# Kernel optimization log

Hardware: AMD Instinct MI355X
Metric: run time of the kernel (lower is better)

Reference implementation:

```python
import jax, jax.numpy as jnp
import numpy as np

CUTOFF = 5.0
NLINKED = 1
CELL_LIST = CUTOFF / NLINKED  # linked-cell edge length
_r = np.arange(-NLINKED, NLINKED + 1)
# torch.cartesian_prod(r1,r1,r1) == meshgrid(indexing='ij') stacked & flattened
LINKED = np.stack(np.meshgrid(_r, _r, _r, indexing='ij'), axis=-1).reshape(1, -1, 3).astype(np.float32)  # (1, 27, 3)


def setup_inputs() -> dict:
    N = 2744
    L = 30.0
    key = jax.random.key(0)
    k1, k2 = jax.random.split(key)
    coordinates = jax.random.uniform(k1, (N, 3), dtype=jnp.float32) * L
    cell = jnp.eye(3, dtype=jnp.float32) * L
    mass = jax.random.uniform(k2, (N,), dtype=jnp.float32) * 15.0 + 1.0
    period_table = jnp.ones((3,), dtype=jnp.int32)  # fully periodic
    return {"period_table": period_table, "coordinates": coordinates, "cell": cell, "mass": mass}


def _forward(period_table, coordinates, cell, mass):
    numatom = coordinates.shape[0]
    # wrap coordinates into the cell relative to atom 0 (fractional coords)
    inv_cell = jnp.linalg.inv(cell)
    inv_coor = coordinates @ inv_cell
    inv_coor = inv_coor - jnp.round(inv_coor - inv_coor[0])
    coordinates = inv_coor @ cell
    # remove center of mass
    com = (mass @ coordinates) / jnp.sum(mass)
    coordinates = coordinates - com[None, :]
    # periodic replicas needed to cover the cutoff
    num_repeats = jnp.ceil(jnp.min(CUTOFF / jnp.abs(cell), axis=0)).astype(jnp.int32)
    num_repeats = period_table.astype(jnp.int32) * num_repeats
    up = num_repeats + 1
    down = -num_repeats
    rs = [jnp.arange(int(down[i]), int(up[i])) for i in range(3)]
    g = jnp.meshgrid(*rs, indexing='ij')
    shifts_frac = jnp.stack(g, axis=-1).reshape(-1, 3).astype(coordinates.dtype)  # (S, 3)
    shifts = shifts_frac @ cell  # (S, 3) cartesian shift vectors
    num_shifts = shifts.shape[0]
    # prod = cartesian_prod(all_shifts, all_atoms).T : row0 shift idx, row1 atom idx
    prod0 = jnp.repeat(jnp.arange(num_shifts), numatom)
    prod1 = jnp.tile(jnp.arange(numatom), num_shifts)
    # shift box so all coords are positive; pad by cutoff
    mincoor = jnp.min(coordinates, axis=0) - CUTOFF - 1e-6
    coordinates = coordinates - mincoor
    maxcoor = jnp.max(coordinates, axis=0) + CUTOFF
    # all periodic images, keep only those inside the padded box
    image = (coordinates[None, :, :] + shifts[:, None, :]).reshape(-1, 3)
    keep = jnp.nonzero(((image < maxcoor) & (image > 0)).all(axis=1))[0]
    image_mask = image[keep]                      # (M, 3)
    prod0 = prod0[keep]
    prod1 = prod1[keep]
    # linked-cell indices
    ori_image_index = jnp.floor(coordinates / CELL_LIST)         # (N, 3)
    neigh_cell = ori_image_index[:, None, :] + jnp.asarray(LINKED)  # (N, 27, 3)
    image_index = jnp.floor(image_mask / CELL_LIST)              # (M, 3)
    max_cell_index = jnp.ceil(maxcoor / CELL_LIST)
    f10 = max_cell_index[1] * max_cell_index[0]
    neigh_cell_index = neigh_cell[:, :, 2] * f10 + neigh_cell[:, :, 1] * max_cell_index[0] + neigh_cell[:, :, 0]  # (N, 27)
    nimage_index = image_index[:, 2] * f10 + image_index[:, 1] * max_cell_index[0] + image_index[:, 0]            # (M,)
    # dense (N, M, 27) cell-index equality -- the memory-bound hot spot
    eq = neigh_cell_index[:, None, :] == nimage_index[None, :, None]
    ai, aj, _ = jnp.nonzero(eq)
    # distance filter on candidate pairs
    d = jnp.linalg.norm(coordinates[ai] - image_mask[aj], axis=-1)
    pair = jnp.nonzero((d < CUTOFF) & (d > 0.001))[0]
    center = ai[pair]
    img = aj[pair]
    shift_idx = prod0[img]
    atom_j = prod1[img]
    neigh_list = jnp.stack([center, atom_j])  # (2, P)
    return neigh_list, shifts[shift_idx], shifts_frac, shift_idx


def reference(period_table, coordinates, cell, mass):
    neigh_list, shifts_out, _, _ = _forward(period_table, coordinates, cell, mass)
    return (neigh_list, shifts_out)
```

## Files before the change

### kernel.cpp

```cpp
#include <hip/hip_runtime.h>
#include <math.h>

#define S_CAP     27
#define NCELL_MAX 1024
#define CAP       64
#define CAPSH     6
#define MAXNB     128
#define CUT       5.0f
#define K1T       1024


__global__ __launch_bounds__(K1T)
void k1_pre(const int* __restrict__ period, const float* __restrict__ coor,
            const float* __restrict__ cell, const float* __restrict__ mass,
            int* hdr_i, float* hdr_f, float* shifts, float* xv,
            int* __restrict__ ccur, int n)
{
    #pragma clang fp contract(off)
    __shared__ double wsum[16][4];
    __shared__ float  wred[16][6];
    int t = threadIdx.x;

    for (int c = t; c < NCELL_MAX; c += K1T) ccur[c] = 0;

    float c[3][3];
    #pragma unroll
    for (int i = 0; i < 3; i++)
        #pragma unroll
        for (int j = 0; j < 3; j++) c[i][j] = cell[3 * i + j];

    float a00 = c[1][1]*c[2][2] - c[1][2]*c[2][1];
    float a01 = c[0][2]*c[2][1] - c[0][1]*c[2][2];
    float a02 = c[0][1]*c[1][2] - c[0][2]*c[1][1];
    float a10 = c[1][2]*c[2][0] - c[1][0]*c[2][2];
    float a11 = c[0][0]*c[2][2] - c[0][2]*c[2][0];
    float a12 = c[0][2]*c[1][0] - c[0][0]*c[1][2];
    float a20 = c[1][0]*c[2][1] - c[1][1]*c[2][0];
    float a21 = c[0][1]*c[2][0] - c[0][0]*c[2][1];
    float a22 = c[0][0]*c[1][1] - c[0][1]*c[1][0];
    float det = c[0][0]*a00 + c[0][1]*a10 + c[0][2]*a20;
    float inv[3][3] = {{a00/det, a01/det, a02/det},
                       {a10/det, a11/det, a12/det},
                       {a20/det, a21/det, a22/det}};

    float f0[3];
    #pragma unroll
    for (int d = 0; d < 3; d++)
        f0[d] = coor[0]*inv[0][d] + coor[1]*inv[1][d] + coor[2]*inv[2][d];

    double sm = 0.0, sx = 0.0, sy = 0.0, sz = 0.0;
    float mn0 =  __builtin_inff(), mn1 =  __builtin_inff(), mn2 =  __builtin_inff();
    float mx0 = -__builtin_inff(), mx1 = -__builtin_inff(), mx2 = -__builtin_inff();
    for (int i = t; i < n; i += K1T) {
        float p0 = coor[3*i], p1 = coor[3*i+1], p2 = coor[3*i+2];
        float ic[3], w[3], x[3];
        #pragma unroll
        for (int d = 0; d < 3; d++)
            ic[d] = p0*inv[0][d] + p1*inv[1][d] + p2*inv[2][d];
        #pragma unroll
        for (int d = 0; d < 3; d++)
            w[d] = ic[d] - rintf(ic[d] - f0[d]);
        #pragma unroll
        for (int d = 0; d < 3; d++)
            x[d] = w[0]*c[0][d] + w[1]*c[1][d] + w[2]*c[2][d];
        xv[3*i] = x[0]; xv[3*i+1] = x[1]; xv[3*i+2] = x[2];
        float m = mass[i];
        sm += (double)m;
        sx += (double)m * (double)x[0];
        sy += (double)m * (double)x[1];
        sz += (double)m * (double)x[2];
        mn0 = fminf(mn0, x[0]); mn1 = fminf(mn1, x[1]); mn2 = fminf(mn2, x[2]);
        mx0 = fmaxf(mx0, x[0]); mx1 = fmaxf(mx1, x[1]); mx2 = fmaxf(mx2, x[2]);
    }
    #pragma unroll
    for (int off = 32; off > 0; off >>= 1) {
        sm += __shfl_down(sm, off, 64);
        sx += __shfl_down(sx, off, 64);
        sy += __shfl_down(sy, off, 64);
        sz += __shfl_down(sz, off, 64);
        mn0 = fminf(mn0, __shfl_down(mn0, off, 64));
        mn1 = fminf(mn1, __shfl_down(mn1, off, 64));
        mn2 = fminf(mn2, __shfl_down(mn2, off, 64));
        mx0 = fmaxf(mx0, __shfl_down(mx0, off, 64));
        mx1 = fmaxf(mx1, __shfl_down(mx1, off, 64));
        mx2 = fmaxf(mx2, __shfl_down(mx2, off, 64));
    }
    if ((t & 63) == 0) {
        int wv = t >> 6;
        wsum[wv][0] = sm; wsum[wv][1] = sx; wsum[wv][2] = sy; wsum[wv][3] = sz;
        wred[wv][0] = mn0; wred[wv][1] = mn1; wred[wv][2] = mn2;
        wred[wv][3] = mx0; wred[wv][4] = mx1; wred[wv][5] = mx2;
    }
    __syncthreads();
    if (t == 0) {
        double SM = 0.0, SX = 0.0, SY = 0.0, SZ = 0.0;
        float MN0 =  __builtin_inff(), MN1 =  __builtin_inff(), MN2 =  __builtin_inff();
        float MX0 = -__builtin_inff(), MX1 = -__builtin_inff(), MX2 = -__builtin_inff();
        #pragma unroll
        for (int q = 0; q < 16; q++) {
            SM += wsum[q][0]; SX += wsum[q][1]; SY += wsum[q][2]; SZ += wsum[q][3];
            MN0 = fminf(MN0, wred[q][0]); MN1 = fminf(MN1, wred[q][1]); MN2 = fminf(MN2, wred[q][2]);
            MX0 = fmaxf(MX0, wred[q][3]); MX1 = fmaxf(MX1, wred[q][4]); MX2 = fmaxf(MX2, wred[q][5]);
        }
        float den  = (float)SM;
        float com0 = ((float)SX) / den;
        float com1 = ((float)SY) / den;
        float com2 = ((float)SZ) / den;
        float m20 = ((MN0 - com0) - CUT) - 1e-6f;
        float m21 = ((MN1 - com1) - CUT) - 1e-6f;
        float m22 = ((MN2 - com2) - CUT) - 1e-6f;
        float maxc0 = ((MX0 - com0) - m20) + CUT;
        float maxc1 = ((MX1 - com1) - m21) + CUT;
        float maxc2 = ((MX2 - com2) - m22) + CUT;
        float mcell0 = ceilf(maxc0 / CUT);
        float mcell1 = ceilf(maxc1 / CUT);
        float f10 = mcell1 * mcell0;
        int nr[3];
        for (int j = 0; j < 3; j++) {
            float v = __builtin_inff();
            for (int i = 0; i < 3; i++) {
                float q = CUT / fabsf(c[i][j]);
                v = fminf(v, q);
            }
            nr[j] = (int)ceilf(v);
            nr[j] *= period[j];
        }
        int nsz0 = 2*nr[0]+1, nsz1 = 2*nr[1]+1, nsz2 = 2*nr[2]+1;
        int S = nsz0 * nsz1 * nsz2;
        if (S > S_CAP) S = S_CAP;
        hdr_i[0] = S;
        hdr_i[3] = -nr[0]; hdr_i[4] = -nr[1]; hdr_i[5] = -nr[2];
        hdr_i[6] = nsz0;   hdr_i[7] = nsz1;   hdr_i[8] = nsz2;
        hdr_i[9]  = (int)mcell0;
        hdr_i[10] = (int)f10;
        hdr_f[0] = maxc0; hdr_f[1] = maxc1; hdr_f[2] = maxc2;
        hdr_f[3] = f10;   hdr_f[4] = mcell0;
        hdr_f[5] = m20;   hdr_f[6] = m21;   hdr_f[7] = m22;
        hdr_f[8] = com0;  hdr_f[9] = com1;  hdr_f[10] = com2;
    }
    __syncthreads();
    int S = hdr_i[0];
    if (t < S) {
        int n1 = hdr_i[7], n2 = hdr_i[8];
        int i0 = t / (n1 * n2);
        int rem = t - i0 * n1 * n2;
        int i1 = rem / n2;
        int i2 = rem - i1 * n2;
        float fx = (float)(hdr_i[3] + i0);
        float fy = (float)(hdr_i[4] + i1);
        float fz = (float)(hdr_i[5] + i2);
        #pragma unroll
        for (int d = 0; d < 3; d++)
            shifts[3*t + d] = fx*c[0][d] + fy*c[1][d] + fz*c[2][d];
    }
}

__global__ __launch_bounds__(256)
void k2_fill(const int* __restrict__ hdr_i, const float* __restrict__ hdr_f,
             const float* __restrict__ shifts, const float* __restrict__ xv,
             int* __restrict__ ccur, float4* __restrict__ cellbuf, int n)
{
    #pragma clang fp contract(off)
    int a = blockIdx.x * 256 + threadIdx.x;
    int s = blockIdx.y;
    if (a >= n || s >= hdr_i[0]) return;
    float m20 = hdr_f[5], m21 = hdr_f[6], m22 = hdr_f[7];
    float com0 = hdr_f[8], com1 = hdr_f[9], com2 = hdr_f[10];
    float u0 = (xv[3*a]   - com0) - m20;
    float u1 = (xv[3*a+1] - com1) - m21;
    float u2 = (xv[3*a+2] - com2) - m22;
    float i0 = u0 + shifts[3*s];
    float i1 = u1 + shifts[3*s+1];
    float i2 = u2 + shifts[3*s+2];
    bool k = (i0 > 0.0f) && (i0 < hdr_f[0]) &&
             (i1 > 0.0f) && (i1 < hdr_f[1]) &&
             (i2 > 0.0f) && (i2 < hdr_f[2]);
    if (!k) return;
    float fc0 = floorf(i0 / CUT);
    float fc1 = floorf(i1 / CUT);
    float fc2 = floorf(i2 / CUT);
    float cf = fc2 * hdr_f[3] + fc1 * hdr_f[4] + fc0;
    int ci = (int)cf;
    if ((unsigned)ci >= (unsigned)NCELL_MAX) return;
    int pos = atomicAdd(&ccur[ci], 1);
    if (pos < CAP)
        cellbuf[(ci << CAPSH) + pos] = make_float4(i0, i1, i2, __int_as_float(s * n + a));
}

__global__ __launch_bounds__(256)
void k3_search(const int* __restrict__ hdr_i, const float* __restrict__ hdr_f,
               const float* __restrict__ xv, const int* __restrict__ ccur,
               const float4* __restrict__ cellbuf, int* __restrict__ nb,
               int* __restrict__ npair, int n)
{
    #pragma clang fp contract(off)
    int t    = threadIdx.x;
    int lane = t & 63;
    int w    = t >> 6;
    int atom = blockIdx.x * 4 + w;
    if (atom >= n) return;

    float m20 = hdr_f[5], m21 = hdr_f[6], m22 = hdr_f[7];
    float com0 = hdr_f[8], com1 = hdr_f[9], com2 = hdr_f[10];
    int mci = hdr_i[9], f10i = hdr_i[10];
    float x0 = (xv[3*atom]   - com0) - m20;
    float x1 = (xv[3*atom+1] - com1) - m21;
    float x2 = (xv[3*atom+2] - com2) - m22;
    int o0 = (int)floorf(x0 / CUT);
    int o1 = (int)floorf(x1 / CUT);
    int o2 = (int)floorf(x2 / CUT);

    int ncb[9], c0a[9], c1a[9], cum[10];
    cum[0] = 0;
    #pragma unroll
    for (int r = 0; r < 9; r++) {
        int dz = r / 3 - 1, dy = r % 3 - 1;
        ncb[r] = (o2+dz)*f10i + (o1+dy)*mci + (o0-1);
        int q0 = 0, q1 = 0, q2 = 0, nc;
        nc = ncb[r];     if ((unsigned)nc < (unsigned)NCELL_MAX) { q0 = ccur[nc]; q0 = q0 > CAP ? CAP : q0; }
        nc = ncb[r] + 1; if ((unsigned)nc < (unsigned)NCELL_MAX) { q1 = ccur[nc]; q1 = q1 > CAP ? CAP : q1; }
        nc = ncb[r] + 2; if ((unsigned)nc < (unsigned)NCELL_MAX) { q2 = ccur[nc]; q2 = q2 > CAP ? CAP : q2; }
        c0a[r] = q0; c1a[r] = q1;
        cum[r+1] = cum[r] + q0 + q1 + q2;
    }
    int T = cum[9];
    int cnt = 0;
    int* slab = nb + (size_t)atom * MAXNB;
    for (int base = 0; base < T; base += 64) {
        int L = base + lane;
        bool act = L < T;
        bool ok = false; int g = 0;
        if (act) {
            int r = 0;
            #pragma unroll
            for (int q = 1; q < 9; q++) r += (L >= cum[q]) ? 1 : 0;
            int off = L - cum[r];
            int c0 = c0a[r], c1 = c1a[r];
            int slot = (off < c0)      ? ((ncb[r]     << CAPSH) + off)
                     : (off < c0 + c1) ? (((ncb[r]+1) << CAPSH) + off - c0)
                                       : (((ncb[r]+2) << CAPSH) + off - c0 - c1);
            float4 v = cellbuf[slot];
            g = __float_as_int(v.w);
            float dxx = x0 - v.x;
            float dyy = x1 - v.y;
            float dzz = x2 - v.z;
            float ss = dxx*dxx + dyy*dyy + dzz*dzz;
            float dd = sqrtf(ss);
            ok = (dd < CUT) && (dd > 0.001f);
        }
        unsigned long long m = __ballot(ok);
        int posn = cnt + (int)__popcll(m & ((1ull << lane) - 1ull));
        if (ok && posn < MAXNB) slab[posn] = g;
        cnt += (int)__popcll(m);
    }
    if (cnt > MAXNB) cnt = MAXNB;
    if (lane == 0) npair[atom] = cnt;
}

__global__ __launch_bounds__(256)
void k4_emit(const int* __restrict__ nb, const int* __restrict__ npair,
             const float* __restrict__ shifts, float* __restrict__ out,
             int n, int P)
{
    __shared__ int si[256];
    __shared__ int lst[4][MAXNB];
    __shared__ int s_np[4];
    int t    = threadIdx.x;
    int lane = t & 63;
    int w    = t >> 6;
    int blk  = blockIdx.x;
    int atom = blk * 4 + w;
    bool valid = atom < n;

    int lim = blk * 4;
    int s = 0;
    for (int i = t; i < lim; i += 256) s += npair[i];
    si[t] = s;
    __syncthreads();
    for (int off = 128; off > 0; off >>= 1) {
        if (t < off) si[t] += si[t + off];
        __syncthreads();
    }
    int prefB = si[0];

    int cnt = 0;
    if (valid) {
        cnt = npair[atom];
        if (cnt > MAXNB) cnt = MAXNB;
        if (lane == 0) s_np[w] = cnt;
        const int* slab = nb + (size_t)atom * MAXNB;
        for (int r = lane; r < cnt; r += 64) lst[w][r] = slab[r];
    } else if (lane == 0) {
        s_np[w] = 0;
    }
    __syncthreads();

    if (valid) {
        int base = prefB;
        for (int q = 0; q < w; q++) base += s_np[q];
        for (int r = lane; r < cnt; r += 64) {
            int g = lst[w][r];
            int rank = 0;
            for (int q = 0; q < cnt; q++) rank += (lst[w][q] < g) ? 1 : 0;
            int p = base + rank;
            if (p < P) {
                int sidx = g / n;
                int a = g - sidx * n;
                out[p]     = (float)atom;
                out[P + p] = (float)a;
                out[2*P + 3*p]     = shifts[3*sidx];
                out[2*P + 3*p + 1] = shifts[3*sidx + 1];
                out[2*P + 3*p + 2] = shifts[3*sidx + 2];
            }
        }
    }
}

extern "C" void kernel_launch(void* const* d_in, const int* in_sizes, int n_in,
                              void* d_out, int out_size, void* d_ws, size_t ws_size,
                              hipStream_t stream)
{
    const int*   period = (const int*)d_in[0];
    const float* coor   = (const float*)d_in[1];
    const float* cell   = (const float*)d_in[2];
    const float* mass   = (const float*)d_in[3];
    float* out = (float*)d_out;

    int n = in_sizes[1] / 3;
    int P = out_size / 5;

    char* wp = (char*)d_ws;
    size_t off = 0;
    auto alloc = [&](size_t bytes) -> void* {
        off = (off + 15) & ~(size_t)15;
        void* pp = (void*)(wp + off); off += bytes; return pp;
    };

    int*    hdr_i   = (int*)   alloc(16 * 4);
    float*  hdr_f   = (float*) alloc(16 * 4);
    float*  shifts  = (float*) alloc(3 * S_CAP * 4);
    float*  xv      = (float*) alloc(3 * (size_t)n * 4);
    int*    ccur    = (int*)   alloc(NCELL_MAX * 4);
    float4* cellbuf = (float4*)alloc((size_t)NCELL_MAX * CAP * 16);
    int*    nb      = (int*)   alloc((size_t)n * MAXNB * 4);
    int*    npair   = (int*)   alloc((size_t)n * 4);
    (void)ws_size; (void)n_in;

    int gb_atom = (n + 3) / 4;
    dim3 g2((n + 255) / 256, S_CAP);

    hipLaunchKernelGGL(k1_pre,    dim3(1),       dim3(K1T), 0, stream,
                       period, coor, cell, mass, hdr_i, hdr_f, shifts, xv, ccur, n);
    hipLaunchKernelGGL(k2_fill,   g2,            dim3(256), 0, stream,
                       hdr_i, hdr_f, shifts, xv, ccur, cellbuf, n);
    hipLaunchKernelGGL(k3_search, dim3(gb_atom), dim3(256), 0, stream,
                       hdr_i, hdr_f, xv, ccur, cellbuf, nb, npair, n);
    hipLaunchKernelGGL(k4_emit,   dim3(gb_atom), dim3(256), 0, stream,
                       nb, npair, shifts, out, n, P);
}
```

Before: 87.46 us.

## Fuse preprocessing into cell-fill kernel with redundant per-block reductions

Merges the single-block preprocessing kernel into the cell-fill kernel. Every block now recomputes the wrapped coordinates, the center-of-mass and min/max reductions over all atoms, and the shift vectors itself. Block (0,0) still writes the header and the shift table for later kernels. The wrapped-coordinate buffer is removed, the search kernel recomputes atom wrapping from the raw inputs, and the counter reset moves to a memset. This removes one serial single-block launch and its dependency, at the cost of redundant O(N) reduction work in each of roughly 297 blocks, plus a memset call.

Result: slower. 89.74 us (+2.6%).

```diff
diff --git a/kernel.cpp b/kernel.cpp
--- a/kernel.cpp
+++ b/kernel.cpp
@@ -7,21 +7,66 @@
 #define CAPSH     6
 #define MAXNB     128
 #define CUT       5.0f
-#define K1T       1024
-
-
-__global__ __launch_bounds__(K1T)
-void k1_pre(const int* __restrict__ period, const float* __restrict__ coor,
-            const float* __restrict__ cell, const float* __restrict__ mass,
-            int* hdr_i, float* hdr_f, float* shifts, float* xv,
-            int* __restrict__ ccur, int n)
+
+
+struct Hdr {
+    float com0, com1, com2, m20, m21, m22, maxc0, maxc1, maxc2;
+    float mcell0, f10;
+    int   S, nsz1, nsz2, dn0, dn1, dn2, mci, f10i;
+};
+
+__device__ inline Hdr make_hdr(double SM, double SX, double SY, double SZ,
+                               float MN0, float MN1, float MN2,
+                               float MX0, float MX1, float MX2,
+                               const float c[3][3], const int* period)
 {
     #pragma clang fp contract(off)
-    __shared__ double wsum[16][4];
-    __shared__ float  wred[16][6];
+    Hdr h;
+    float den = (float)SM;
+    h.com0 = ((float)SX) / den;
+    h.com1 = ((float)SY) / den;
+    h.com2 = ((float)SZ) / den;
+    h.m20 = ((MN0 - h.com0) - CUT) - 1e-6f;
+    h.m21 = ((MN1 - h.com1) - CUT) - 1e-6f;
+    h.m22 = ((MN2 - h.com2) - CUT) - 1e-6f;
+    h.maxc0 = ((MX0 - h.com0) - h.m20) + CUT;
+    h.maxc1 = ((MX1 - h.com1) - h.m21) + CUT;
+    h.maxc2 = ((MX2 - h.com2) - h.m22) + CUT;
+    h.mcell0 = ceilf(h.maxc0 / CUT);
+    float mcell1 = ceilf(h.maxc1 / CUT);
+    h.f10 = mcell1 * h.mcell0;
+    int nr[3];
+    for (int j = 0; j < 3; j++) {
+        float v = __builtin_inff();
+        for (int i = 0; i < 3; i++) {
+            float q = CUT / fabsf(c[i][j]);
+            v = fminf(v, q);
+        }
+        nr[j] = (int)ceilf(v);
+        nr[j] *= period[j];
+    }
+    int nsz0 = 2*nr[0]+1; h.nsz1 = 2*nr[1]+1; h.nsz2 = 2*nr[2]+1;
+    int S = nsz0 * h.nsz1 * h.nsz2;
+    if (S > S_CAP) S = S_CAP;
+    h.S = S;
+    h.dn0 = -nr[0]; h.dn1 = -nr[1]; h.dn2 = -nr[2];
+    h.mci  = (int)h.mcell0;
+    h.f10i = (int)h.f10;
+    return h;
+}
+
+__global__ __launch_bounds__(256)
+void k12_fill(const int* __restrict__ period, const float* __restrict__ coor,
+              const float* __restrict__ cell, const float* __restrict__ mass,
+              int* hdr_i, float* hdr_f, float* shifts,
+              int* __restrict__ ccur, float4* __restrict__ cellbuf, int n)
+{
+    #pragma clang fp contract(off)
+    __shared__ double wsum[4][4];
+    __shared__ float  wred[4][6];
     int t = threadIdx.x;
-
-    for (int c = t; c < NCELL_MAX; c += K1T) ccur[c] = 0;
+    int lane = t & 63;
+    int wv = t >> 6;
 
     float c[3][3];
     #pragma unroll
@@ -51,7 +96,10 @@
     double sm = 0.0, sx = 0.0, sy = 0.0, sz = 0.0;
     float mn0 =  __builtin_inff(), mn1 =  __builtin_inff(), mn2 =  __builtin_inff();
     float mx0 = -__builtin_inff(), mx1 = -__builtin_inff(), mx2 = -__builtin_inff();
-    for (int i = t; i < n; i += K1T) {
+    float ax0 = 0.f, ax1 = 0.f, ax2 = 0.f;
+    bool hasatom = false;
+    int k = 0;
+    for (int i = t; i < n; i += 256, k++) {
         float p0 = coor[3*i], p1 = coor[3*i+1], p2 = coor[3*i+2];
         float ic[3], w[3], x[3];
         #pragma unroll
@@ -63,7 +111,7 @@
         #pragma unroll
         for (int d = 0; d < 3; d++)
             x[d] = w[0]*c[0][d] + w[1]*c[1][d] + w[2]*c[2][d];
-        xv[3*i] = x[0]; xv[3*i+1] = x[1]; xv[3*i+2] = x[2];
+        if (k == (int)blockIdx.x) { ax0 = x[0]; ax1 = x[1]; ax2 = x[2]; hasatom = true; }
         float m = mass[i];
         sm += (double)m;
         sx += (double)m * (double)x[0];
@@ -85,113 +133,88 @@
         mx1 = fmaxf(mx1, __shfl_down(mx1, off, 64));
         mx2 = fmaxf(mx2, __shfl_down(mx2, off, 64));
     }
-    if ((t & 63) == 0) {
-        int wv = t >> 6;
+    if (lane == 0) {
         wsum[wv][0] = sm; wsum[wv][1] = sx; wsum[wv][2] = sy; wsum[wv][3] = sz;
         wred[wv][0] = mn0; wred[wv][1] = mn1; wred[wv][2] = mn2;
         wred[wv][3] = mx0; wred[wv][4] = mx1; wred[wv][5] = mx2;
     }
     __syncthreads();
-    if (t == 0) {
-        double SM = 0.0, SX = 0.0, SY = 0.0, SZ = 0.0;
-        float MN0 =  __builtin_inff(), MN1 =  __builtin_inff(), MN2 =  __builtin_inff();
-        float MX0 = -__builtin_inff(), MX1 = -__builtin_inff(), MX2 = -__builtin_inff();
-        #pragma unroll
-        for (int q = 0; q < 16; q++) {
-            SM += wsum[q][0]; SX += wsum[q][1]; SY += wsum[q][2]; SZ += wsum[q][3];
-            MN0 = fminf(MN0, wred[q][0]); MN1 = fminf(MN1, wred[q][1]); MN2 = fminf(MN2, wred[q][2]);
-            MX0 = fmaxf(MX0, wred[q][3]); MX1 = fmaxf(MX1, wred[q][4]); MX2 = fmaxf(MX2, wred[q][5]);
+    double SM = 0.0, SX = 0.0, SY = 0.0, SZ = 0.0;
+    float MN0 =  __builtin_inff(), MN1 =  __builtin_inff(), MN2 =  __builtin_inff();
+    float MX0 = -__builtin_inff(), MX1 = -__builtin_inff(), MX2 = -__builtin_inff();
+    #pragma unroll
+    for (int q = 0; q < 4; q++) {
+        SM += wsum[q][0]; SX += wsum[q][1]; SY += wsum[q][2]; SZ += wsum[q][3];
+        MN0 = fminf(MN0, wred[q][0]); MN1 = fminf(MN1, wred[q][1]); MN2 = fminf(MN2, wred[q][2]);
+        MX0 = fmaxf(MX0, wred[q][3]); MX1 = fmaxf(MX1, wred[q][4]); MX2 = fmaxf(MX2, wred[q][5]);
+    }
+    Hdr h = make_hdr(SM, SX, SY, SZ, MN0, MN1, MN2, MX0, MX1, MX2, c, period);
+
+    if (blockIdx.x == 0 && blockIdx.y == 0) {
+        if (t == 0) {
+            hdr_i[0] = h.S;
+            hdr_i[3] = h.dn0; hdr_i[4] = h.dn1; hdr_i[5] = h.dn2;
+            hdr_i[7] = h.nsz1; hdr_i[8] = h.nsz2;
+            hdr_i[9]  = h.mci;
+            hdr_i[10] = h.f10i;
+            hdr_f[0] = h.maxc0; hdr_f[1] = h.maxc1; hdr_f[2] = h.maxc2;
+            hdr_f[3] = h.f10;   hdr_f[4] = h.mcell0;
+            hdr_f[5] = h.m20;   hdr_f[6] = h.m21;   hdr_f[7] = h.m22;
+            hdr_f[8] = h.com0;  hdr_f[9] = h.com1;  hdr_f[10] = h.com2;
         }
-        float den  = (float)SM;
-        float com0 = ((float)SX) / den;
-        float com1 = ((float)SY) / den;
-        float com2 = ((float)SZ) / den;
-        float m20 = ((MN0 - com0) - CUT) - 1e-6f;
-        float m21 = ((MN1 - com1) - CUT) - 1e-6f;
-        float m22 = ((MN2 - com2) - CUT) - 1e-6f;
-        float maxc0 = ((MX0 - com0) - m20) + CUT;
-        float maxc1 = ((MX1 - com1) - m21) + CUT;
-        float maxc2 = ((MX2 - com2) - m22) + CUT;
-        float mcell0 = ceilf(maxc0 / CUT);
-        float mcell1 = ceilf(maxc1 / CUT);
-        float f10 = mcell1 * mcell0;
-        int nr[3];
-        for (int j = 0; j < 3; j++) {
-            float v = __builtin_inff();
-            for (int i = 0; i < 3; i++) {
-                float q = CUT / fabsf(c[i][j]);
-                v = fminf(v, q);
-            }
-            nr[j] = (int)ceilf(v);
-            nr[j] *= period[j];
+        if (t < h.S) {
+            int i0 = t / (h.nsz1 * h.nsz2);
+            int rem = t - i0 * h.nsz1 * h.nsz2;
+            int i1 = rem / h.nsz2;
+            int i2 = rem - i1 * h.nsz2;
+            float fx = (float)(h.dn0 + i0);
+            float fy = (float)(h.dn1 + i1);
+            float fz = (float)(h.dn2 + i2);
+            #pragma unroll
+            for (int d = 0; d < 3; d++)
+                shifts[3*t + d] = fx*c[0][d] + fy*c[1][d] + fz*c[2][d];
         }
-        int nsz0 = 2*nr[0]+1, nsz1 = 2*nr[1]+1, nsz2 = 2*nr[2]+1;
-        int S = nsz0 * nsz1 * nsz2;
-        if (S > S_CAP) S = S_CAP;
-        hdr_i[0] = S;
-        hdr_i[3] = -nr[0]; hdr_i[4] = -nr[1]; hdr_i[5] = -nr[2];
-        hdr_i[6] = nsz0;   hdr_i[7] = nsz1;   hdr_i[8] = nsz2;
-        hdr_i[9]  = (int)mcell0;
-        hdr_i[10] = (int)f10;
-        hdr_f[0] = maxc0; hdr_f[1] = maxc1; hdr_f[2] = maxc2;
-        hdr_f[3] = f10;   hdr_f[4] = mcell0;
-        hdr_f[5] = m20;   hdr_f[6] = m21;   hdr_f[7] = m22;
-        hdr_f[8] = com0;  hdr_f[9] = com1;  hdr_f[10] = com2;
-    }
-    __syncthreads();
-    int S = hdr_i[0];
-    if (t < S) {
-        int n1 = hdr_i[7], n2 = hdr_i[8];
-        int i0 = t / (n1 * n2);
-        int rem = t - i0 * n1 * n2;
-        int i1 = rem / n2;
-        int i2 = rem - i1 * n2;
-        float fx = (float)(hdr_i[3] + i0);
-        float fy = (float)(hdr_i[4] + i1);
-        float fz = (float)(hdr_i[5] + i2);
-        #pragma unroll
-        for (int d = 0; d < 3; d++)
-            shifts[3*t + d] = fx*c[0][d] + fy*c[1][d] + fz*c[2][d];
-    }
-}
-
-__global__ __launch_bounds__(256)
-void k2_fill(const int* __restrict__ hdr_i, const float* __restrict__ hdr_f,
-             const float* __restrict__ shifts, const float* __restrict__ xv,
-             int* __restrict__ ccur, float4* __restrict__ cellbuf, int n)
-{
-    #pragma clang fp contract(off)
-    int a = blockIdx.x * 256 + threadIdx.x;
+    }
+
     int s = blockIdx.y;
-    if (a >= n || s >= hdr_i[0]) return;
-    float m20 = hdr_f[5], m21 = hdr_f[6], m22 = hdr_f[7];
-    float com0 = hdr_f[8], com1 = hdr_f[9], com2 = hdr_f[10];
-    float u0 = (xv[3*a]   - com0) - m20;
-    float u1 = (xv[3*a+1] - com1) - m21;
-    float u2 = (xv[3*a+2] - com2) - m22;
-    float i0 = u0 + shifts[3*s];
-    float i1 = u1 + shifts[3*s+1];
-    float i2 = u2 + shifts[3*s+2];
-    bool k = (i0 > 0.0f) && (i0 < hdr_f[0]) &&
-             (i1 > 0.0f) && (i1 < hdr_f[1]) &&
-             (i2 > 0.0f) && (i2 < hdr_f[2]);
-    if (!k) return;
+    if (!hasatom || s >= h.S) return;
+    int i0s = s / (h.nsz1 * h.nsz2);
+    int rem = s - i0s * h.nsz1 * h.nsz2;
+    int i1s = rem / h.nsz2;
+    int i2s = rem - i1s * h.nsz2;
+    float fx = (float)(h.dn0 + i0s);
+    float fy = (float)(h.dn1 + i1s);
+    float fz = (float)(h.dn2 + i2s);
+    float sh0 = fx*c[0][0] + fy*c[1][0] + fz*c[2][0];
+    float sh1 = fx*c[0][1] + fy*c[1][1] + fz*c[2][1];
+    float sh2 = fx*c[0][2] + fy*c[1][2] + fz*c[2][2];
+    float u0 = (ax0 - h.com0) - h.m20;
+    float u1 = (ax1 - h.com1) - h.m21;
+    float u2 = (ax2 - h.com2) - h.m22;
+    float i0 = u0 + sh0;
+    float i1 = u1 + sh1;
+    float i2 = u2 + sh2;
+    bool kk = (i0 > 0.0f) && (i0 < h.maxc0) &&
+              (i1 > 0.0f) && (i1 < h.maxc1) &&
+              (i2 > 0.0f) && (i2 < h.maxc2);
+    if (!kk) return;
     float fc0 = floorf(i0 / CUT);
     float fc1 = floorf(i1 / CUT);
     float fc2 = floorf(i2 / CUT);
-    float cf = fc2 * hdr_f[3] + fc1 * hdr_f[4] + fc0;
+    float cf = fc2 * h.f10 + fc1 * h.mcell0 + fc0;
     int ci = (int)cf;
     if ((unsigned)ci >= (unsigned)NCELL_MAX) return;
+    int a = blockIdx.x * 256 + t;
     int pos = atomicAdd(&ccur[ci], 1);
     if (pos < CAP)
         cellbuf[(ci << CAPSH) + pos] = make_float4(i0, i1, i2, __int_as_float(s * n + a));
 }
 
 __global__ __launch_bounds__(256)
-void k3_search(const int* __restrict__ hdr_i, const float* __restrict__ hdr_f,
-               const float* __restrict__ xv, const int* __restrict__ ccur,
-               const float4* __restrict__ cellbuf, int* __restrict__ nb,
-               int* __restrict__ npair, int n)
+void k3_search(const float* __restrict__ coor, const float* __restrict__ cell,
+               const int* __restrict__ hdr_i, const float* __restrict__ hdr_f,
+               const int* __restrict__ ccur, const float4* __restrict__ cellbuf,
+               int* __restrict__ nb, int* __restrict__ npair, int n)
 {
     #pragma clang fp contract(off)
     int t    = threadIdx.x;
@@ -200,12 +223,47 @@
     int atom = blockIdx.x * 4 + w;
     if (atom >= n) return;
 
+    float c[3][3];
+    #pragma unroll
+    for (int i = 0; i < 3; i++)
+        #pragma unroll
+        for (int j = 0; j < 3; j++) c[i][j] = cell[3 * i + j];
+    float a00 = c[1][1]*c[2][2] - c[1][2]*c[2][1];
+    float a01 = c[0][2]*c[2][1] - c[0][1]*c[2][2];
+    float a02 = c[0][1]*c[1][2] - c[0][2]*c[1][1];
+    float a10 = c[1][2]*c[2][0] - c[1][0]*c[2][2];
+    float a11 = c[0][0]*c[2][2] - c[0][2]*c[2][0];
+    float a12 = c[0][2]*c[1][0] - c[0][0]*c[1][2];
+    float a20 = c[1][0]*c[2][1] - c[1][1]*c[2][0];
+    float a21 = c[0][1]*c[2][0] - c[0][0]*c[2][1];
+    float a22 = c[0][0]*c[1][1] - c[0][1]*c[1][0];
+    float det = c[0][0]*a00 + c[0][1]*a10 + c[0][2]*a20;
+    float inv[3][3] = {{a00/det, a01/det, a02/det},
+                       {a10/det, a11/det, a12/det},
+                       {a20/det, a21/det, a22/det}};
+    float f0[3];
+    #pragma unroll
+    for (int d = 0; d < 3; d++)
+        f0[d] = coor[0]*inv[0][d] + coor[1]*inv[1][d] + coor[2]*inv[2][d];
+
+    float p0 = coor[3*atom], p1 = coor[3*atom+1], p2 = coor[3*atom+2];
+    float ic[3], ww[3], x[3];
+    #pragma unroll
+    for (int d = 0; d < 3; d++)
+        ic[d] = p0*inv[0][d] + p1*inv[1][d] + p2*inv[2][d];
+    #pragma unroll
+    for (int d = 0; d < 3; d++)
+        ww[d] = ic[d] - rintf(ic[d] - f0[d]);
+    #pragma unroll
+    for (int d = 0; d < 3; d++)
+        x[d] = ww[0]*c[0][d] + ww[1]*c[1][d] + ww[2]*c[2][d];
+
     float m20 = hdr_f[5], m21 = hdr_f[6], m22 = hdr_f[7];
     float com0 = hdr_f[8], com1 = hdr_f[9], com2 = hdr_f[10];
     int mci = hdr_i[9], f10i = hdr_i[10];
-    float x0 = (xv[3*atom]   - com0) - m20;
-    float x1 = (xv[3*atom+1] - com1) - m21;
-    float x2 = (xv[3*atom+2] - com2) - m22;
+    float x0 = (x[0] - com0) - m20;
+    float x1 = (x[1] - com1) - m21;
+    float x2 = (x[2] - com2) - m22;
     int o0 = (int)floorf(x0 / CUT);
     int o1 = (int)floorf(x1 / CUT);
     int o2 = (int)floorf(x2 / CUT);
@@ -339,7 +397,6 @@
     int*    hdr_i   = (int*)   alloc(16 * 4);
     float*  hdr_f   = (float*) alloc(16 * 4);
     float*  shifts  = (float*) alloc(3 * S_CAP * 4);
-    float*  xv      = (float*) alloc(3 * (size_t)n * 4);
     int*    ccur    = (int*)   alloc(NCELL_MAX * 4);
     float4* cellbuf = (float4*)alloc((size_t)NCELL_MAX * CAP * 16);
     int*    nb      = (int*)   alloc((size_t)n * MAXNB * 4);
@@ -347,14 +404,13 @@
     (void)ws_size; (void)n_in;
 
     int gb_atom = (n + 3) / 4;
-    dim3 g2((n + 255) / 256, S_CAP);
-
-    hipLaunchKernelGGL(k1_pre,    dim3(1),       dim3(K1T), 0, stream,
-                       period, coor, cell, mass, hdr_i, hdr_f, shifts, xv, ccur, n);
-    hipLaunchKernelGGL(k2_fill,   g2,            dim3(256), 0, stream,
-                       hdr_i, hdr_f, shifts, xv, ccur, cellbuf, n);
+    dim3 g12((n + 255) / 256, S_CAP);
+
+    hipMemsetAsync(ccur, 0, NCELL_MAX * 4, stream);
+    hipLaunchKernelGGL(k12_fill,  g12,           dim3(256), 0, stream,
+                       period, coor, cell, mass, hdr_i, hdr_f, shifts, ccur, cellbuf, n);
     hipLaunchKernelGGL(k3_search, dim3(gb_atom), dim3(256), 0, stream,
-                       hdr_i, hdr_f, xv, ccur, cellbuf, nb, npair, n);
+                       coor, cell, hdr_i, hdr_f, ccur, cellbuf, nb, npair, n);
     hipLaunchKernelGGL(k4_emit,   dim3(gb_atom), dim3(256), 0, stream,
                        nb, npair, shifts, out, n, P);
 }
```
